# Optimization experiments

Hardware: AMD Instinct MI355X
Metric: run time of the kernel (lower is better)

Reference implementation:

```python
import jax, jax.numpy as jnp
import numpy as np

VOCAB = 50257
EXTRA = 64          # static over-approximation of num_oovs
SEQ = 1024
T_DEC = 100
E = 128
H = 160             # encoder hidden per direction; decoder hidden = 2H = 320
UNK = 3
START = 0
NEG = -1e9


def lstm_cell(x, h, c, wih, whh, bih, bhh):
    # torch gate order: i, f, g, o
    g = x @ wih.T + h @ whh.T + bih + bhh
    i, f, gg, o = jnp.split(g, 4, axis=-1)
    c = jax.nn.sigmoid(f) * c + jax.nn.sigmoid(i) * jnp.tanh(gg)
    h = jax.nn.sigmoid(o) * jnp.tanh(c)
    return h, c


def run_lstm(xs, wih, whh, bih, bhh, hdim):
    def step(carry, x):
        h, c = carry
        h, c = lstm_cell(x, h, c, wih, whh, bih, bhh)
        return (h, c), h
    init = (jnp.zeros((hdim,), xs.dtype), jnp.zeros((hdim,), xs.dtype))
    (hf, _), hs = jax.lax.scan(step, init, xs)
    return hs, hf


def setup_inputs() -> dict:
    key = jax.random.key(0)
    ks = jax.random.split(key, 20)
    rn = lambda k, shape, s: (jax.random.normal(k, shape, dtype=jnp.float32) * s)
    inp = {
        'input_ids': jax.random.randint(ks[0], (SEQ,), 0, VOCAB + EXTRA),
        'embedding': rn(ks[1], (VOCAB, E), 0.1),
        'enc_wih_f': rn(ks[2], (4 * H, E), 0.08),
        'enc_whh_f': rn(ks[3], (4 * H, H), 0.08),
        'enc_bih_f': rn(ks[4], (4 * H,), 0.05),
        'enc_bhh_f': rn(ks[5], (4 * H,), 0.05),
        'enc_wih_b': rn(ks[6], (4 * H, E), 0.08),
        'enc_whh_b': rn(ks[7], (4 * H, H), 0.08),
        'enc_bih_b': rn(ks[8], (4 * H,), 0.05),
        'enc_bhh_b': rn(ks[9], (4 * H,), 0.05),
        'dec_wih': rn(ks[10], (8 * H, E), 0.08),
        'dec_whh': rn(ks[11], (8 * H, 2 * H), 0.08),
        'dec_bih': rn(ks[12], (8 * H,), 0.05),
        'dec_bhh': rn(ks[13], (8 * H,), 0.05),
        'enc_attn_proj': rn(ks[14], (2 * H, 2 * H), 0.02),
        'dec_attn_proj': rn(ks[15], (2 * H, 2 * H), 0.02),
        'vocab_proj': rn(ks[16], (E, 6 * H), 0.05),
        'out_bias': rn(ks[17], (VOCAB,), 0.01),
        'switch_w': rn(ks[18], (1, 6 * H), 0.05),
        'switch_b': rn(ks[19], (1,), 0.05),
    }
    return inp


def reference(input_ids, embedding, enc_wih_f, enc_whh_f, enc_bih_f, enc_bhh_f,
              enc_wih_b, enc_whh_b, enc_bih_b, enc_bhh_b,
              dec_wih, dec_whh, dec_bih, dec_bhh,
              enc_attn_proj, dec_attn_proj, vocab_proj, out_bias,
              switch_w, switch_b):
    ids_in = jnp.where(input_ids >= VOCAB, UNK, input_ids)
    emb = embedding[ids_in]                               # [S, E]

    # bidirectional encoder LSTM
    h_fwd, hfin_f = run_lstm(emb, enc_wih_f, enc_whh_f, enc_bih_f, enc_bhh_f, H)
    h_bwd_rev, hfin_b = run_lstm(emb[::-1], enc_wih_b, enc_whh_b, enc_bih_b, enc_bhh_b, H)
    enc_h = jnp.concatenate([h_fwd, h_bwd_rev[::-1]], axis=-1)   # [S, 2H]

    # step-invariant vocab projection: tanh(W_emb @ vocab_proj) -> [V, 6H]
    out_proj = jnp.tanh(embedding @ vocab_proj)

    # precompute projected encoder states for attention: [S, 2H]
    enc_proj_h = enc_h @ enc_attn_proj.T

    h0 = jnp.concatenate([hfin_f, hfin_b])                # [2H]
    c0 = jnp.zeros((2 * H,), enc_h.dtype)
    dec_buf0 = jnp.zeros((T_DEC, 2 * H), enc_h.dtype)
    cum0 = jnp.zeros((SEQ,), enc_h.dtype)
    tok0 = jnp.asarray(START, dtype=input_ids.dtype)
    t_range = jnp.arange(T_DEC)

    def step(carry, t):
        h, c, cum, dec_buf, tok = carry
        x = embedding[jnp.where(tok >= VOCAB, UNK, tok)]
        h, c = lstm_cell(x, h, c, dec_wih, dec_whh, dec_bih, dec_bhh)

        # intra-temporal encoder attention
        scores = enc_proj_h @ h                           # [S] = h @ W_e @ enc_h.T
        cum_safe = jnp.where(t == 0, 1.0, cum)
        temporal = jnp.where(t == 0, scores, jnp.exp(scores) / cum_safe)
        attn = jax.nn.softmax(temporal)
        enc_ctx = attn @ enc_h                            # [2H]

        # intra-decoder attention over previous decoder hidden states
        dscores = (h @ dec_attn_proj) @ dec_buf.T         # [T_DEC]
        dmask = t_range < t
        dattn = jax.nn.softmax(jnp.where(dmask, dscores, NEG))
        dec_ctx = jnp.where(t == 0, jnp.zeros_like(h), dattn @ dec_buf)

        concat = jnp.concatenate([h, enc_ctx, dec_ctx])   # [6H]
        vocab_dist = jax.nn.softmax(out_proj @ concat + out_bias)  # [V]
        p_copy = jax.nn.sigmoid(jnp.dot(switch_w[0], concat) + switch_b[0])
        gen = jnp.pad((1.0 - p_copy) * vocab_dist, (0, EXTRA))     # [V+EXTRA]
        final = gen.at[input_ids].add(p_copy * attn)      # pointer scatter-add

        cum = cum + scores
        dec_buf = dec_buf.at[t].set(h)
        tok = jnp.argmax(final).astype(input_ids.dtype)   # greedy decode
        return (h, c, cum, dec_buf, tok), final

    _, finals = jax.lax.scan(step, (h0, c0, cum0, dec_buf0, tok0), t_range)
    return finals                                         # [T_DEC, V+EXTRA]
```

## Files before the change

### kernel.cpp

```cpp
#include <hip/hip_runtime.h>
#include <cstdint>

#define VOCAB 50257
#define VTOT  50321
#define TDEC  100
#define UNK   3
#define NBLK  256
#define NTHR  512
#define VB0   17
#define NVB   197
#define K4N   120

static const size_t OFF_WT     = 0;
static const size_t OFF_EMB    = 0;
static const size_t OFF_WIHT_F = 131072;
static const size_t OFF_WIHT_B = 212992;
static const size_t OFF_WTE    = 294912;
static const size_t OFF_XG     = 397312;
static const size_t OFF_ENCH   = 24207360;
static const size_t OFF_EPH    = 24535040;
static const size_t OFF_DECBUF = 24862720;
static const size_t OFF_GATES  = 24894720;
static const size_t OFF_HPAR   = 24896000;
static const size_t OFF_CPAR   = 24898560;
static const size_t OFF_DCTX   = 24903680;
static const size_t OFF_H0     = 24904000;
static const size_t OFF_TEMP   = 24904320;
static const size_t OFF_ATTN   = 24905344;
static const size_t OFF_PMS    = 24906368;
static const size_t OFF_BM     = 24906880;
static const size_t OFF_BS     = 24907136;
static const size_t OFF_AVAL   = 24907392;
static const size_t OFF_AIDX   = 24907648;
static const size_t OFF_PC     = 24907904;
static const size_t OFF_BAR    = 24907968;
static const size_t OFF_SKEY   = 24908032;
static const size_t OFF_SPOS   = 24909056;
static const size_t OFF_BSTART = 24910080;

__device__ __forceinline__ float sigmf(float x) { return 1.f / (1.f + expf(-x)); }

__device__ __forceinline__ float wsum64(float x) {
#pragma unroll
  for (int m = 1; m < 64; m <<= 1) x += __shfl_xor(x, m, 64);
  return x;
}

__device__ __forceinline__ unsigned short bf16r(float x) {
  uint32_t b = __float_as_uint(x);
  uint32_t r = (b + 0x7fffu + ((b >> 16) & 1u)) >> 16;
  return (unsigned short)r;
}
__device__ __forceinline__ float bflo(unsigned u) { return __uint_as_float(u << 16); }
__device__ __forceinline__ float bfhi(unsigned u) { return __uint_as_float(u & 0xffff0000u); }

__device__ __forceinline__ float cload(const float* p) {
  return __hip_atomic_load((float*)p, __ATOMIC_RELAXED, __HIP_MEMORY_SCOPE_AGENT);
}
__device__ __forceinline__ void cstore(float* p, float v) {
  __hip_atomic_store(p, v, __ATOMIC_RELAXED, __HIP_MEMORY_SCOPE_AGENT);
}
__device__ __forceinline__ int cloadi(const int* p) {
  return __hip_atomic_load((int*)p, __ATOMIC_RELAXED, __HIP_MEMORY_SCOPE_AGENT);
}
__device__ __forceinline__ void cstorei(int* p, int v) {
  __hip_atomic_store(p, v, __ATOMIC_RELAXED, __HIP_MEMORY_SCOPE_AGENT);
}

__device__ __forceinline__ void gridbar(float* ws) {
  int* bar = (int*)(ws + OFF_BAR);
  __syncthreads();
  if (threadIdx.x == 0) {
    asm volatile("s_waitcnt vmcnt(0) lgkmcnt(0)" ::: "memory");
    int g = __hip_atomic_load(&bar[32], __ATOMIC_RELAXED, __HIP_MEMORY_SCOPE_AGENT);
    int old = __hip_atomic_fetch_add(&bar[0], 1, __ATOMIC_RELAXED, __HIP_MEMORY_SCOPE_AGENT);
    if (old == NBLK - 1) {
      __hip_atomic_store(&bar[0], 0, __ATOMIC_RELAXED, __HIP_MEMORY_SCOPE_AGENT);
      __hip_atomic_store(&bar[32], g + 1, __ATOMIC_RELAXED, __HIP_MEMORY_SCOPE_AGENT);
    } else {
      while (__hip_atomic_load(&bar[32], __ATOMIC_RELAXED, __HIP_MEMORY_SCOPE_AGENT) == g)
        __builtin_amdgcn_s_sleep(2);
    }
  }
  __syncthreads();
}

__global__ __launch_bounds__(256) void k_setup(float* __restrict__ ws, const int* __restrict__ ids,
                                               const float* __restrict__ embt, const float* __restrict__ ewf,
                                               const float* __restrict__ ewb, const float* __restrict__ eap) {
  int idx = blockIdx.x * 256 + threadIdx.x;
  if (idx < 131072) {
    int tt = idx >> 7, e = idx & 127;
    int id = ids[tt]; if (id >= VOCAB) id = UNK;
    ws[OFF_EMB + idx] = embt[(size_t)id * 128 + e];
  } else if (idx < 212992) {
    int i = idx - 131072;
    int k = i / 640, g = i - (i / 640) * 640;
    ws[OFF_WIHT_F + i] = ewf[(size_t)g * 128 + k];
  } else if (idx < 294912) {
    int i = idx - 212992;
    int k = i / 640, g = i - (i / 640) * 640;
    ws[OFF_WIHT_B + i] = ewb[(size_t)g * 128 + k];
  } else if (idx < 397312) {
    int i = idx - 294912;
    int k = i / 320, j = i - (i / 320) * 320;
    ws[OFF_WTE + i] = eap[(size_t)j * 320 + k];
  }
}

__global__ __launch_bounds__(256) void k_xg(float* __restrict__ ws,
                                            const float* __restrict__ bif, const float* __restrict__ bhf,
                                            const float* __restrict__ bib, const float* __restrict__ bhb) {
  int idx = blockIdx.x * 256 + threadIdx.x;
  int d = idx / 655360;
  int r = idx - d * 655360;
  int tt = r / 640, g = r - (r / 640) * 640;
  const float* wT = ws + (d ? OFF_WIHT_B : OFF_WIHT_F);
  const float* er = ws + OFF_EMB + (size_t)(d ? (1023 - tt) : tt) * 128;
  float acc = d ? (bib[g] + bhb[g]) : (bif[g] + bhf[g]);
#pragma unroll 4
  for (int k = 0; k < 128; ++k) acc += er[k] * wT[(size_t)k * 640 + g];
  ws[OFF_XG + idx] = acc;
}

__global__ __launch_bounds__(512) void k_encoder(float* __restrict__ ws, const float* __restrict__ whh_f,
                                                 const float* __restrict__ whh_b) {
  const int dir = blockIdx.x;
  const int tid = threadIdx.x;
  const float* whh = dir ? whh_b : whh_f;
  const float* xg = ws + OFF_XG + (size_t)dir * 655360;
  __shared__ float hbuf[160];
  __shared__ float part[4][640];
  const int q = tid & 127, kg = tid >> 7, ks = kg * 40;
  float w[5][40];
#pragma unroll
  for (int j = 0; j < 5; ++j)
#pragma unroll
    for (int i = 0; i < 40; ++i)
      w[j][i] = whh[(size_t)(5 * q + j) * 160 + ks + i];
  float cst = 0.f;
  if (tid < 160) hbuf[tid] = 0.f;
  __syncthreads();
  for (int t = 0; t < 1024; ++t) {
    float acc[5] = {0.f, 0.f, 0.f, 0.f, 0.f};
#pragma unroll
    for (int i4 = 0; i4 < 10; ++i4) {
      float4 h4 = *(const float4*)&hbuf[ks + i4 * 4];
#pragma unroll
      for (int j = 0; j < 5; ++j)
        acc[j] += w[j][i4 * 4 + 0] * h4.x + w[j][i4 * 4 + 1] * h4.y + w[j][i4 * 4 + 2] * h4.z + w[j][i4 * 4 + 3] * h4.w;
    }
#pragma unroll
    for (int j = 0; j < 5; ++j) part[kg][5 * q + j] = acc[j];
    __syncthreads();
    if (tid < 160) {
      float gi = xg[(size_t)t * 640 + tid];
      float gf = xg[(size_t)t * 640 + 160 + tid];
      float gg = xg[(size_t)t * 640 + 320 + tid];
      float go = xg[(size_t)t * 640 + 480 + tid];
#pragma unroll
      for (int k2 = 0; k2 < 4; ++k2) {
        gi += part[k2][tid]; gf += part[k2][160 + tid];
        gg += part[k2][320 + tid]; go += part[k2][480 + tid];
      }
      cst = sigmf(gf) * cst + sigmf(gi) * tanhf(gg);
      float hn = sigmf(go) * tanhf(cst);
      hbuf[tid] = hn;
      int trow = dir ? (1023 - t) : t;
      ws[OFF_ENCH + (size_t)trow * 320 + dir * 160 + tid] = hn;
    }
    __syncthreads();
  }
  if (tid < 160) ws[OFF_H0 + dir * 160 + tid] = hbuf[tid];
}

__global__ __launch_bounds__(256) void k_encproj(float* __restrict__ ws) {
  int idx = blockIdx.x * 256 + threadIdx.x;
  int s = idx / 320, j = idx - (idx / 320) * 320;
  const float* er = ws + OFF_ENCH + (size_t)s * 320;
  const float* wt = ws + OFF_WTE;
  float acc = 0.f;
#pragma unroll 4
  for (int k = 0; k < 320; ++k) acc += er[k] * wt[(size_t)k * 320 + j];
  ws[OFF_EPH + idx] = acc;
}

__global__ __launch_bounds__(256) void k_outproj(const float* __restrict__ embt, const float* __restrict__ vp,
                                                 float* __restrict__ ws) {
  __shared__ float As[64][128];
  __shared__ float Bs[128][64];
  __shared__ unsigned T[32][64];
  const int tid = threadIdx.x;
  const int v0 = blockIdx.x * 64, n0 = blockIdx.y * 64;
  for (int c = 0; c < 32; ++c) {
    int idx = c * 256 + tid;
    int m = idx >> 7, k = idx & 127;
    int v = v0 + m;
    As[m][k] = (v < VOCAB) ? embt[(size_t)v * 128 + k] : 0.f;
    int k2 = idx >> 6, n = idx & 63;
    Bs[k2][n] = vp[(size_t)k2 * 960 + n0 + n];
  }
  __syncthreads();
  const int mi = tid >> 4, ni = tid & 15;
  float acc[4][4] = {};
  for (int k = 0; k < 128; ++k) {
    float a0 = As[mi * 4 + 0][k], a1 = As[mi * 4 + 1][k], a2 = As[mi * 4 + 2][k], a3 = As[mi * 4 + 3][k];
    float4 b = *(const float4*)&Bs[k][ni * 4];
    acc[0][0] += a0 * b.x; acc[0][1] += a0 * b.y; acc[0][2] += a0 * b.z; acc[0][3] += a0 * b.w;
    acc[1][0] += a1 * b.x; acc[1][1] += a1 * b.y; acc[1][2] += a1 * b.z; acc[1][3] += a1 * b.w;
    acc[2][0] += a2 * b.x; acc[2][1] += a2 * b.y; acc[2][2] += a2 * b.z; acc[2][3] += a2 * b.w;
    acc[3][0] += a3 * b.x; acc[3][1] += a3 * b.y; acc[3][2] += a3 * b.z; acc[3][3] += a3 * b.w;
  }
#pragma unroll
  for (int i = 0; i < 4; ++i) {
    unsigned p0 = (unsigned)bf16r(tanhf(acc[i][0])) | ((unsigned)bf16r(tanhf(acc[i][1])) << 16);
    unsigned p1 = (unsigned)bf16r(tanhf(acc[i][2])) | ((unsigned)bf16r(tanhf(acc[i][3])) << 16);
    T[2 * ni][mi * 4 + i] = p0;
    T[2 * ni + 1][mi * 4 + i] = p1;
  }
  __syncthreads();
  uint4* WT4 = (uint4*)(ws + OFF_WT);
  const int vb = blockIdx.x >> 2;
  const int rb = (blockIdx.x & 3) * 64;
  const int k4b = n0 >> 3;
#pragma unroll
  for (int i = 0; i < 2; ++i) {
    int flat = i * 256 + tid;
    int k4l = flat >> 6, col = flat & 63;
    uint4 u;
    u.x = T[4 * k4l + 0][col];
    u.y = T[4 * k4l + 1][col];
    u.z = T[4 * k4l + 2][col];
    u.w = T[4 * k4l + 3][col];
    WT4[(size_t)vb * (K4N * 256) + (size_t)(k4b + k4l) * 256 + rb + col] = u;
  }
}

__global__ __launch_bounds__(512) void k_sort(float* __restrict__ ws, const int* __restrict__ ids) {
  __shared__ int sk[1024], sp[1024];
  const int tid = threadIdx.x;
  for (int j = tid; j < 1024; j += 512) { sk[j] = ids[j]; sp[j] = j; }
  __syncthreads();
  for (int k = 2; k <= 1024; k <<= 1)
    for (int j = k >> 1; j > 0; j >>= 1) {
      for (int i = tid; i < 1024; i += 512) {
        int ixj = i ^ j;
        if (ixj > i) {
          bool up = ((i & k) == 0);
          int a = sk[i], b2 = sk[ixj];
          if (up ? (a > b2) : (a < b2)) {
            sk[i] = b2; sk[ixj] = a;
            int pa = sp[i]; sp[i] = sp[ixj]; sp[ixj] = pa;
          }
        }
      }
      __syncthreads();
    }
  int* BST = (int*)(ws + OFF_BSTART);
  int* SK = (int*)(ws + OFF_SKEY);
  int* SP = (int*)(ws + OFF_SPOS);
  for (int j = tid; j < 1024; j += 512) {
    SK[j] = sk[j]; SP[j] = sp[j];
    int o1 = sk[j] >> 8;
    int o0 = (j == 0) ? -1 : (sk[j - 1] >> 8);
    for (int o = o0 + 1; o <= o1; ++o) BST[o] = j;
  }
  if (tid < 256) {
    ws[OFF_AVAL + tid] = -1e30f;
    ((int*)(ws + OFF_AIDX))[tid] = 0;
    ws[OFF_BM + tid] = -1e30f;
    ws[OFF_BS + tid] = 0.f;
  }
  if (tid == 0) {
    int olast = sk[1023] >> 8;
    for (int o = olast + 1; o <= NVB; ++o) BST[o] = 1024;
    int* bar = (int*)(ws + OFF_BAR);
    bar[0] = 0; bar[32] = 0;
  }
}

__global__ __launch_bounds__(512) void k_decode(float* __restrict__ ws, float* __restrict__ out,
    const float* __restrict__ embt,
    const float* __restrict__ dwih, const float* __restrict__ dwhh,
    const float* __restrict__ dbih, const float* __restrict__ dbhh,
    const float* __restrict__ dap, const float* __restrict__ sw,
    const float* __restrict__ sb, const float* __restrict__ ob) {
  const int b = blockIdx.x, tid = threadIdx.x;
  const int l = tid & 63, w = tid >> 6;
  const int rl = tid & 255, half = tid >> 8;
  const int vb = b - VB0;
  const bool isv = (vb >= 0) && (vb < NVB);
  const int vrow = isv ? (vb * 256 + rl) : 0;
  const bool myrow = isv && (vrow < VOCAB);
  const uint4* WTb = ((const uint4*)(ws + OFF_WT)) + (size_t)(isv ? vb : 0) * (K4N * 256) + rl;

  __shared__ __align__(16) float hL[320];
  __shared__ float cL[320];
  __shared__ __align__(16) float concatL[960];
  __shared__ float logitsL[256];
  __shared__ float p0L[256], p1L[256];
  __shared__ float tauL[4], cumL[4];
  __shared__ float redA[512], redB[512];
  __shared__ int   redI[512];
  __shared__ float attnL[64], dsL[128], daL[128], hpL[320];

  if (tid < 320) { hL[tid] = ws[OFF_H0 + tid]; cL[tid] = 0.f; }
  if (tid < 4) cumL[tid] = 0.f;
  __syncthreads();

  for (int t = 0; t < TDEC; ++t) {
    int token = 0;
    if (t > 0) {
      float av = -1e30f; int ai = 0;
      if (tid < 256) { av = cload(&ws[OFF_AVAL + tid]); ai = cloadi(((const int*)(ws + OFF_AIDX)) + tid); }
      redA[tid] = av; redI[tid] = ai;
      __syncthreads();
      for (int off = 256; off > 0; off >>= 1) {
        if (tid < off) {
          float v2 = redA[tid + off]; int i2 = redI[tid + off];
          if (v2 > redA[tid] || (v2 == redA[tid] && i2 < redI[tid])) { redA[tid] = v2; redI[tid] = i2; }
        }
        __syncthreads();
      }
      token = redI[0];
    }
    int tokm = (token >= VOCAB) ? UNK : token;
    if (w < 5) {
      const int r = 5 * b + w;
      float acc = dwih[(size_t)r * 128 + l] * embt[(size_t)tokm * 128 + l]
                + dwih[(size_t)r * 128 + 64 + l] * embt[(size_t)tokm * 128 + 64 + l];
#pragma unroll
      for (int c = 0; c < 5; ++c) acc += dwhh[(size_t)r * 320 + c * 64 + l] * hL[c * 64 + l];
      acc = wsum64(acc);
      if (l == 0) cstore(&ws[OFF_GATES + r], acc + dbih[r] + dbhh[r]);
    }
    gridbar(ws);

    if (tid < 320) {
      float gi = cload(&ws[OFF_GATES + tid]);
      float gf = cload(&ws[OFF_GATES + 320 + tid]);
      float gg = cload(&ws[OFF_GATES + 640 + tid]);
      float go = cload(&ws[OFF_GATES + 960 + tid]);
      float c = sigmf(gf) * cL[tid] + sigmf(gi) * tanhf(gg);
      cL[tid] = c;
      float hn = sigmf(go) * tanhf(c);
      hL[tid] = hn;
      if (b == 16) ws[OFF_DECBUF + (size_t)t * 320 + tid] = hn;
    }
    __syncthreads();
    if (w < 4) {
      const int srow = 4 * b + w;
      const float* er = ws + OFF_EPH + (size_t)srow * 320;
      float acc = 0.f;
#pragma unroll
      for (int c = 0; c < 5; ++c) acc += er[c * 64 + l] * hL[c * 64 + l];
      acc = wsum64(acc);
      float tau = (t == 0) ? acc : expf(acc) / cumL[w];
      if (l == 0) {
        tauL[w] = tau;
        cstore(&ws[OFF_TEMP + srow], tau);
        cumL[w] += acc;
      }
    }
    if (b < 8 && tid < 320) {
      float acc = 0.f;
#pragma unroll 8
      for (int ii = 0; ii < 40; ++ii) {
        int i = b * 40 + ii;
        acc += hL[i] * dap[(size_t)i * 320 + tid];
      }
      cstore(&ws[OFF_HPAR + b * 320 + tid], acc);
    }
    __syncthreads();
    if (tid == 0) {
      float m4 = fmaxf(fmaxf(tauL[0], tauL[1]), fmaxf(tauL[2], tauL[3]));
      float s4 = expf(tauL[0] - m4) + expf(tauL[1] - m4) + expf(tauL[2] - m4) + expf(tauL[3] - m4);
      cstore(&ws[OFF_PMS + 2 * b], m4);
      cstore(&ws[OFF_PMS + 2 * b + 1], s4);
    }
    gridbar(ws);

    float ga0 = 0.f, ga1 = 0.f;
    if (b < 16) {
      float m = -1e30f, s = 0.f;
      if (tid < 256) { m = cload(&ws[OFF_PMS + 2 * tid]); s = cload(&ws[OFF_PMS + 2 * tid + 1]); }
      redA[tid] = m; redB[tid] = s;
      __syncthreads();
      for (int off = 256; off > 0; off >>= 1) {
        if (tid < off) {
          float m1 = redA[tid], m2 = redA[tid + off];
          float mx = fmaxf(m1, m2);
          redB[tid] = redB[tid] * expf(m1 - mx) + redB[tid + off] * expf(m2 - mx);
          redA[tid] = mx;
        }
        __syncthreads();
      }
      const float M = redA[0], S = redB[0];
      __syncthreads();
      if (tid < 64) {
        float a = expf(cload(&ws[OFF_TEMP + 64 * b + tid]) - M) / S;
        attnL[tid] = a;
        cstore(&ws[OFF_ATTN + 64 * b + tid], a);
      }
      __syncthreads();
      if (tid < 320) {
        float acc = 0.f;
        const float* eh = ws + OFF_ENCH + (size_t)(64 * b) * 320 + tid;
#pragma unroll 4
        for (int k2 = 0; k2 < 64; ++k2) acc += attnL[k2] * eh[(size_t)k2 * 320];
        cstore(&ws[OFF_CPAR + b * 320 + tid], acc);
      }
    } else if (b == 16) {
      if (tid < 320) {
        float a = 0.f;
#pragma unroll
        for (int q = 0; q < 8; ++q) a += cload(&ws[OFF_HPAR + q * 320 + tid]);
        hpL[tid] = a;
      }
      __syncthreads();
      float hpv[5];
#pragma unroll
      for (int c = 0; c < 5; ++c) hpv[c] = hpL[c * 64 + l];
#pragma unroll
      for (int k2 = 0; k2 < 13; ++k2) {
        int tp = w + 8 * k2;
        if (tp < t) {
          float acc = 0.f;
#pragma unroll
          for (int c = 0; c < 5; ++c) acc += hpv[c] * ws[OFF_DECBUF + (size_t)tp * 320 + c * 64 + l];
          acc = wsum64(acc);
          if (l == 0) dsL[tp] = acc;
        }
      }
      __syncthreads();
      float dv = -1e30f;
      if (tid < 128) { dv = (tid < t) ? dsL[tid] : -1e30f; redA[tid] = dv; }
      __syncthreads();
      for (int off = 64; off > 0; off >>= 1) { if (tid < off) redA[tid] = fmaxf(redA[tid], redA[tid + off]); __syncthreads(); }
      float dmx = redA[0];
      __syncthreads();
      float de = (tid < 128) ? expf(dv - dmx) : 0.f;
      if (tid < 128) redA[tid] = de;
      __syncthreads();
      for (int off = 64; off > 0; off >>= 1) { if (tid < off) redA[tid] += redA[tid + off]; __syncthreads(); }
      float dS = redA[0];
      __syncthreads();
      if (tid < 128) daL[tid] = de / dS;
      __syncthreads();
      if (tid < 320) {
        float acc = 0.f;
        for (int tp = 0; tp < t; ++tp) acc += daL[tp] * ws[OFF_DECBUF + (size_t)tp * 320 + tid];
        cstore(&ws[OFF_DCTX + tid], (t == 0) ? 0.f : acc);
      }
    } else if (isv) {
      const int c0 = half ? 20 : 0;
#pragma unroll 10
      for (int k4 = c0; k4 < c0 + 20; ++k4) {
        uint4 u = WTb[(size_t)k4 * 256];
        float4 fa = *(const float4*)&hL[8 * k4];
        float4 fb = *(const float4*)&hL[8 * k4 + 4];
        ga0 += bflo(u.x) * fa.x + bflo(u.y) * fa.z + bflo(u.z) * fb.x + bflo(u.w) * fb.z;
        ga1 += bfhi(u.x) * fa.y + bfhi(u.y) * fa.w + bfhi(u.z) * fb.y + bfhi(u.w) * fb.w;
      }
    }
    gridbar(ws);

    if (isv || b == 0) {
      if (tid < 320) {
        float e = 0.f;
#pragma unroll
        for (int g2 = 0; g2 < 16; ++g2) e += cload(&ws[OFF_CPAR + g2 * 320 + tid]);
        concatL[tid] = hL[tid];
        concatL[320 + tid] = e;
        concatL[640 + tid] = cload(&ws[OFF_DCTX + tid]);
      }
    }
    __syncthreads();
    if (b == 0 && w == 0) {
      float acc = 0.f;
#pragma unroll
      for (int c = 0; c < 15; ++c) acc += sw[c * 64 + l] * concatL[c * 64 + l];
      acc = wsum64(acc);
      if (l == 0) cstore(&ws[OFF_PC], 1.f / (1.f + expf(-(acc + sb[0]))));
    }
    if (isv) {
      const int d0 = half ? 80 : 40;
#pragma unroll 8
      for (int k4 = d0; k4 < d0 + 40; ++k4) {
        uint4 u = WTb[(size_t)k4 * 256];
        float4 fa = *(const float4*)&concatL[8 * k4];
        float4 fb = *(const float4*)&concatL[8 * k4 + 4];
        ga0 += bflo(u.x) * fa.x + bflo(u.y) * fa.z + bflo(u.z) * fb.x + bflo(u.w) * fb.z;
        ga1 += bfhi(u.x) * fa.y + bfhi(u.y) * fa.w + bfhi(u.z) * fb.y + bfhi(u.w) * fb.w;
      }
      if (half) p1L[rl] = ga0 + ga1; else p0L[rl] = ga0 + ga1;
    }
    __syncthreads();
    float lm = -1e30f, ls = 0.f;
    if (isv && tid < 256) {
      float lv = myrow ? (p0L[tid] + p1L[tid] + ob[vrow]) : -1e30f;
      logitsL[tid] = lv;
      if (lv > -1e29f) { lm = lv; ls = 1.f; }
    }
    redA[tid] = lm; redB[tid] = ls;
    __syncthreads();
    for (int off = 256; off > 0; off >>= 1) {
      if (tid < off) {
        float m1 = redA[tid], m2 = redA[tid + off];
        float mx = fmaxf(m1, m2);
        redB[tid] = redB[tid] * expf(m1 - mx) + redB[tid + off] * expf(m2 - mx);
        redA[tid] = mx;
      }
      __syncthreads();
    }
    if (isv && tid == 0) { cstore(&ws[OFF_BM + vb], redA[0]); cstore(&ws[OFF_BS + vb], redB[0]); }
    gridbar(ws);

    if (isv) {
      float m = -1e30f, s = 0.f;
      if (tid < 256) { m = cload(&ws[OFF_BM + tid]); s = cload(&ws[OFF_BS + tid]); }
      redA[tid] = m; redB[tid] = s;
      __syncthreads();
      for (int off = 256; off > 0; off >>= 1) {
        if (tid < off) {
          float m1 = redA[tid], m2 = redA[tid + off];
          float mx = fmaxf(m1, m2);
          redB[tid] = redB[tid] * expf(m1 - mx) + redB[tid + off] * expf(m2 - mx);
          redA[tid] = mx;
        }
        __syncthreads();
      }
      const float M = redA[0], Sg = redB[0];
      const float pc = cload(&ws[OFF_PC]);
      const float scale = (1.f - pc) / Sg;
      __syncthreads();
      const int* BST = (const int*)(ws + OFF_BSTART);
      const int* SK = (const int*)(ws + OFF_SKEY);
      const int* SP = (const int*)(ws + OFF_SPOS);
      bool act = (tid < 256) && (vrow < VTOT);
      float val = -1e30f;
      if (act) {
        val = (vrow < VOCAB) ? scale * expf(logitsL[tid] - M) : 0.f;
        int jb = BST[vb], je = BST[vb + 1];
        for (int j = jb; j < je; ++j)
          if (SK[j] == vrow) val += pc * cload(&ws[OFF_ATTN + SP[j]]);
        out[(size_t)t * VTOT + vrow] = val;
      }
      redA[tid] = act ? val : -1e30f; redI[tid] = vrow;
      __syncthreads();
      for (int off = 256; off > 0; off >>= 1) {
        if (tid < off) {
          float v2 = redA[tid + off]; int i2 = redI[tid + off];
          if (v2 > redA[tid] || (v2 == redA[tid] && i2 < redI[tid])) { redA[tid] = v2; redI[tid] = i2; }
        }
        __syncthreads();
      }
      if (tid == 0) { cstore(&ws[OFF_AVAL + b], redA[0]); cstorei(((int*)(ws + OFF_AIDX)) + b, redI[0]); }
    }
    gridbar(ws);
  }
}

extern "C" void kernel_launch(void* const* d_in, const int* in_sizes, int n_in,
                              void* d_out, int out_size, void* d_ws, size_t ws_size,
                              hipStream_t stream) {
  const int*   ids  = (const int*)d_in[0];
  const float* embt = (const float*)d_in[1];
  const float* ewf  = (const float*)d_in[2];
  const float* ehf  = (const float*)d_in[3];
  const float* ebif = (const float*)d_in[4];
  const float* ebhf = (const float*)d_in[5];
  const float* ewb  = (const float*)d_in[6];
  const float* ehb  = (const float*)d_in[7];
  const float* ebib = (const float*)d_in[8];
  const float* ebhb = (const float*)d_in[9];
  const float* dwih = (const float*)d_in[10];
  const float* dwhh = (const float*)d_in[11];
  const float* dbih = (const float*)d_in[12];
  const float* dbhh = (const float*)d_in[13];
  const float* eap  = (const float*)d_in[14];
  const float* dap  = (const float*)d_in[15];
  const float* vp   = (const float*)d_in[16];
  const float* ob   = (const float*)d_in[17];
  const float* sw   = (const float*)d_in[18];
  const float* sb   = (const float*)d_in[19];
  float* out = (float*)d_out;
  float* ws  = (float*)d_ws;

  k_setup<<<1558, 256, 0, stream>>>(ws, ids, embt, ewf, ewb, eap);
  k_xg<<<5120, 256, 0, stream>>>(ws, ebif, ebhf, ebib, ebhb);
  k_encoder<<<2, 512, 0, stream>>>(ws, ehf, ehb);
  k_encproj<<<1280, 256, 0, stream>>>(ws);
  k_outproj<<<dim3(786, 15), 256, 0, stream>>>(embt, vp, ws);
  k_sort<<<1, 512, 0, stream>>>(ws, ids);
  k_decode<<<NBLK, NTHR, 0, stream>>>(ws, out, embt, dwih, dwhh, dbih, dbhh, dap, sw, sb, ob);
}
```

Measured before the change: 8.535 ms.

## Spread vocab projection over all blocks, prefetch weights, use hierarchical grid barrier

Reassigns the vocabulary projection so every one of the 256 persistent blocks owns 200 vocab rows, instead of 197 blocks owning 256 rows while 17 blocks do attention and other work. Each block's slice of the bf16 weight layout is loaded into registers before the barriers and attention phases, so weight fetch latency overlaps with other work. The single-counter grid barrier becomes a two-level barrier: 16 groups of 16 blocks each count locally, then one top-level counter releases all groups. This costs more registers per thread and puts vocab work on the attention blocks, which can lengthen their critical path.

```diff
diff --git a/kernel.cpp b/kernel.cpp
--- a/kernel.cpp
+++ b/kernel.cpp
@@ -7,36 +7,36 @@
 #define UNK   3
 #define NBLK  256
 #define NTHR  512
-#define VB0   17
-#define NVB   197
-#define K4N   120
-
-static const size_t OFF_WT     = 0;
+#define VPB   200
+#define NSL   252
+#define K4SL  24000
+
 static const size_t OFF_EMB    = 0;
 static const size_t OFF_WIHT_F = 131072;
 static const size_t OFF_WIHT_B = 212992;
 static const size_t OFF_WTE    = 294912;
 static const size_t OFF_XG     = 397312;
-static const size_t OFF_ENCH   = 24207360;
-static const size_t OFF_EPH    = 24535040;
-static const size_t OFF_DECBUF = 24862720;
-static const size_t OFF_GATES  = 24894720;
-static const size_t OFF_HPAR   = 24896000;
-static const size_t OFF_CPAR   = 24898560;
-static const size_t OFF_DCTX   = 24903680;
-static const size_t OFF_H0     = 24904000;
-static const size_t OFF_TEMP   = 24904320;
-static const size_t OFF_ATTN   = 24905344;
-static const size_t OFF_PMS    = 24906368;
-static const size_t OFF_BM     = 24906880;
-static const size_t OFF_BS     = 24907136;
-static const size_t OFF_AVAL   = 24907392;
-static const size_t OFF_AIDX   = 24907648;
-static const size_t OFF_PC     = 24907904;
-static const size_t OFF_BAR    = 24907968;
-static const size_t OFF_SKEY   = 24908032;
-static const size_t OFF_SPOS   = 24909056;
-static const size_t OFF_BSTART = 24910080;
+static const size_t OFF_WT     = 294912;
+static const size_t OFF_ENCH   = 24486912;
+static const size_t OFF_EPH    = 24814592;
+static const size_t OFF_DECBUF = 25142272;
+static const size_t OFF_GATES  = 25174272;
+static const size_t OFF_HPAR   = 25175552;
+static const size_t OFF_CPAR   = 25178112;
+static const size_t OFF_DCTX   = 25183232;
+static const size_t OFF_H0     = 25183552;
+static const size_t OFF_TEMP   = 25183872;
+static const size_t OFF_ATTN   = 25184896;
+static const size_t OFF_PMS    = 25185920;
+static const size_t OFF_BM     = 25186432;
+static const size_t OFF_BS     = 25186688;
+static const size_t OFF_AVAL   = 25186944;
+static const size_t OFF_AIDX   = 25187200;
+static const size_t OFF_PC     = 25187456;
+static const size_t OFF_BAR    = 25187520;
+static const size_t OFF_SKEY   = 25189568;
+static const size_t OFF_SPOS   = 25190592;
+static const size_t OFF_BSTART = 25191616;
 
 __device__ __forceinline__ float sigmf(float x) { return 1.f / (1.f + expf(-x)); }
 
@@ -67,20 +67,25 @@
   __hip_atomic_store(p, v, __ATOMIC_RELAXED, __HIP_MEMORY_SCOPE_AGENT);
 }
 
-__device__ __forceinline__ void gridbar(float* ws) {
+__device__ __forceinline__ void gridbar(float* ws, int b) {
   int* bar = (int*)(ws + OFF_BAR);
   __syncthreads();
   if (threadIdx.x == 0) {
     asm volatile("s_waitcnt vmcnt(0) lgkmcnt(0)" ::: "memory");
-    int g = __hip_atomic_load(&bar[32], __ATOMIC_RELAXED, __HIP_MEMORY_SCOPE_AGENT);
-    int old = __hip_atomic_fetch_add(&bar[0], 1, __ATOMIC_RELAXED, __HIP_MEMORY_SCOPE_AGENT);
-    if (old == NBLK - 1) {
-      __hip_atomic_store(&bar[0], 0, __ATOMIC_RELAXED, __HIP_MEMORY_SCOPE_AGENT);
-      __hip_atomic_store(&bar[32], g + 1, __ATOMIC_RELAXED, __HIP_MEMORY_SCOPE_AGENT);
-    } else {
-      while (__hip_atomic_load(&bar[32], __ATOMIC_RELAXED, __HIP_MEMORY_SCOPE_AGENT) == g)
-        __builtin_amdgcn_s_sleep(2);
-    }
+    const int g = b >> 4;
+    int* ggen = &bar[512 + g * 32];
+    int myg = __hip_atomic_load(ggen, __ATOMIC_RELAXED, __HIP_MEMORY_SCOPE_AGENT);
+    int old = __hip_atomic_fetch_add(&bar[g * 32], 1, __ATOMIC_RELAXED, __HIP_MEMORY_SCOPE_AGENT);
+    if ((old & 15) == 15) {
+      int r = __hip_atomic_fetch_add(&bar[1024], 1, __ATOMIC_RELAXED, __HIP_MEMORY_SCOPE_AGENT);
+      if ((r & 15) == 15) {
+#pragma unroll
+        for (int i = 0; i < 16; ++i)
+          __hip_atomic_store(&bar[512 + i * 32], myg + 1, __ATOMIC_RELAXED, __HIP_MEMORY_SCOPE_AGENT);
+      }
+    }
+    while (__hip_atomic_load(ggen, __ATOMIC_RELAXED, __HIP_MEMORY_SCOPE_AGENT) == myg)
+      __builtin_amdgcn_s_sleep(1);
   }
   __syncthreads();
 }
@@ -220,19 +225,22 @@
   }
   __syncthreads();
   uint4* WT4 = (uint4*)(ws + OFF_WT);
-  const int vb = blockIdx.x >> 2;
-  const int rb = (blockIdx.x & 3) * 64;
   const int k4b = n0 >> 3;
 #pragma unroll
   for (int i = 0; i < 2; ++i) {
     int flat = i * 256 + tid;
     int k4l = flat >> 6, col = flat & 63;
-    uint4 u;
-    u.x = T[4 * k4l + 0][col];
-    u.y = T[4 * k4l + 1][col];
-    u.z = T[4 * k4l + 2][col];
-    u.w = T[4 * k4l + 3][col];
-    WT4[(size_t)vb * (K4N * 256) + (size_t)(k4b + k4l) * 256 + rb + col] = u;
+    int v = v0 + col;
+    if (v < VOCAB) {
+      int vb = v / VPB;
+      int rl = v - vb * VPB;
+      uint4 u;
+      u.x = T[4 * k4l + 0][col];
+      u.y = T[4 * k4l + 1][col];
+      u.z = T[4 * k4l + 2][col];
+      u.w = T[4 * k4l + 3][col];
+      WT4[(size_t)vb * K4SL + (size_t)(k4b + k4l) * VPB + rl] = u;
+    }
   }
 }
 
@@ -261,10 +269,11 @@
   int* SP = (int*)(ws + OFF_SPOS);
   for (int j = tid; j < 1024; j += 512) {
     SK[j] = sk[j]; SP[j] = sp[j];
-    int o1 = sk[j] >> 8;
-    int o0 = (j == 0) ? -1 : (sk[j - 1] >> 8);
+    int o1 = sk[j] / VPB;
+    int o0 = (j == 0) ? -1 : (sk[j - 1] / VPB);
     for (int o = o0 + 1; o <= o1; ++o) BST[o] = j;
   }
+  for (int j = tid; j < 2048; j += 512) ((int*)(ws + OFF_BAR))[j] = 0;
   if (tid < 256) {
     ws[OFF_AVAL + tid] = -1e30f;
     ((int*)(ws + OFF_AIDX))[tid] = 0;
@@ -272,12 +281,18 @@
     ws[OFF_BS + tid] = 0.f;
   }
   if (tid == 0) {
-    int olast = sk[1023] >> 8;
-    for (int o = olast + 1; o <= NVB; ++o) BST[o] = 1024;
-    int* bar = (int*)(ws + OFF_BAR);
-    bar[0] = 0; bar[32] = 0;
-  }
-}
+    int olast = sk[1023] / VPB;
+    for (int o = olast + 1; o <= 256; ++o) BST[o] = 1024;
+  }
+}
+
+#define LDB(dst, kb) { _Pragma("unroll") for (int j = 0; j < 10; ++j) dst[j] = WTb[(size_t)((kb) + j) * VPB]; }
+#define ACCW(src, kb, CV) { _Pragma("unroll") for (int j = 0; j < 10; ++j) { \
+    const int kk = (kb) + j; \
+    float4 fa = *(const float4*)&CV[8 * kk]; \
+    float4 fb = *(const float4*)&CV[8 * kk + 4]; \
+    ga0 += bflo(src[j].x) * fa.x + bflo(src[j].y) * fa.z + bflo(src[j].z) * fb.x + bflo(src[j].w) * fb.z; \
+    ga1 += bfhi(src[j].x) * fa.y + bfhi(src[j].y) * fa.w + bfhi(src[j].z) * fb.y + bfhi(src[j].w) * fb.w; } }
 
 __global__ __launch_bounds__(512) void k_decode(float* __restrict__ ws, float* __restrict__ out,
     const float* __restrict__ embt,
@@ -288,11 +303,10 @@
   const int b = blockIdx.x, tid = threadIdx.x;
   const int l = tid & 63, w = tid >> 6;
   const int rl = tid & 255, half = tid >> 8;
-  const int vb = b - VB0;
-  const bool isv = (vb >= 0) && (vb < NVB);
-  const int vrow = isv ? (vb * 256 + rl) : 0;
-  const bool myrow = isv && (vrow < VOCAB);
-  const uint4* WTb = ((const uint4*)(ws + OFF_WT)) + (size_t)(isv ? vb : 0) * (K4N * 256) + rl;
+  const int vrow = b * VPB + rl;
+  const bool act = (rl < VPB) && (vrow < VOCAB);
+  const bool hasout = (b * VPB) < VTOT;
+  const uint4* WTb = ((const uint4*)(ws + OFF_WT)) + (size_t)b * K4SL + rl;
 
   __shared__ __align__(16) float hL[320];
   __shared__ float cL[320];
@@ -334,7 +348,7 @@
       acc = wsum64(acc);
       if (l == 0) cstore(&ws[OFF_GATES + r], acc + dbih[r] + dbhh[r]);
     }
-    gridbar(ws);
+    gridbar(ws, b);
 
     if (tid < 320) {
       float gi = cload(&ws[OFF_GATES + tid]);
@@ -378,9 +392,11 @@
       cstore(&ws[OFF_PMS + 2 * b], m4);
       cstore(&ws[OFF_PMS + 2 * b + 1], s4);
     }
-    gridbar(ws);
-
-    float ga0 = 0.f, ga1 = 0.f;
+    gridbar(ws, b);
+
+    uint4 wA[10], wB[10];
+    const int c0 = half ? 20 : 0;
+    if (act) { LDB(wA, c0); LDB(wB, c0 + 10); }
     if (b < 16) {
       float m = -1e30f, s = 0.f;
       if (tid < 256) { m = cload(&ws[OFF_PMS + 2 * tid]); s = cload(&ws[OFF_PMS + 2 * tid + 1]); }
@@ -452,28 +468,20 @@
         for (int tp = 0; tp < t; ++tp) acc += daL[tp] * ws[OFF_DECBUF + (size_t)tp * 320 + tid];
         cstore(&ws[OFF_DCTX + tid], (t == 0) ? 0.f : acc);
       }
-    } else if (isv) {
-      const int c0 = half ? 20 : 0;
-#pragma unroll 10
-      for (int k4 = c0; k4 < c0 + 20; ++k4) {
-        uint4 u = WTb[(size_t)k4 * 256];
-        float4 fa = *(const float4*)&hL[8 * k4];
-        float4 fb = *(const float4*)&hL[8 * k4 + 4];
-        ga0 += bflo(u.x) * fa.x + bflo(u.y) * fa.z + bflo(u.z) * fb.x + bflo(u.w) * fb.z;
-        ga1 += bfhi(u.x) * fa.y + bfhi(u.y) * fa.w + bfhi(u.z) * fb.y + bfhi(u.w) * fb.w;
-      }
-    }
-    gridbar(ws);
-
-    if (isv || b == 0) {
-      if (tid < 320) {
-        float e = 0.f;
-#pragma unroll
-        for (int g2 = 0; g2 < 16; ++g2) e += cload(&ws[OFF_CPAR + g2 * 320 + tid]);
-        concatL[tid] = hL[tid];
-        concatL[320 + tid] = e;
-        concatL[640 + tid] = cload(&ws[OFF_DCTX + tid]);
-      }
+    }
+    float ga0 = 0.f, ga1 = 0.f;
+    if (act) { ACCW(wA, c0, hL); ACCW(wB, c0 + 10, hL); }
+    gridbar(ws, b);
+
+    const int d0 = half ? 80 : 40;
+    if (act) { LDB(wA, d0); LDB(wB, d0 + 10); }
+    if (tid < 320) {
+      float e = 0.f;
+#pragma unroll
+      for (int g2 = 0; g2 < 16; ++g2) e += cload(&ws[OFF_CPAR + g2 * 320 + tid]);
+      concatL[tid] = hL[tid];
+      concatL[320 + tid] = e;
+      concatL[640 + tid] = cload(&ws[OFF_DCTX + tid]);
     }
     __syncthreads();
     if (b == 0 && w == 0) {
@@ -483,43 +491,22 @@
       acc = wsum64(acc);
       if (l == 0) cstore(&ws[OFF_PC], 1.f / (1.f + expf(-(acc + sb[0]))));
     }
-    if (isv) {
-      const int d0 = half ? 80 : 40;
-#pragma unroll 8
-      for (int k4 = d0; k4 < d0 + 40; ++k4) {
-        uint4 u = WTb[(size_t)k4 * 256];
-        float4 fa = *(const float4*)&concatL[8 * k4];
-        float4 fb = *(const float4*)&concatL[8 * k4 + 4];
-        ga0 += bflo(u.x) * fa.x + bflo(u.y) * fa.z + bflo(u.z) * fb.x + bflo(u.w) * fb.z;
-        ga1 += bfhi(u.x) * fa.y + bfhi(u.y) * fa.w + bfhi(u.z) * fb.y + bfhi(u.w) * fb.w;
-      }
+    if (act) {
+      ACCW(wA, d0, concatL); LDB(wA, d0 + 20);
+      ACCW(wB, d0 + 10, concatL); LDB(wB, d0 + 30);
+      ACCW(wA, d0 + 20, concatL);
+      ACCW(wB, d0 + 30, concatL);
       if (half) p1L[rl] = ga0 + ga1; else p0L[rl] = ga0 + ga1;
     }
     __syncthreads();
-    float lm = -1e30f, ls = 0.f;
-    if (isv && tid < 256) {
-      float lv = myrow ? (p0L[tid] + p1L[tid] + ob[vrow]) : -1e30f;
-      logitsL[tid] = lv;
-      if (lv > -1e29f) { lm = lv; ls = 1.f; }
-    }
-    redA[tid] = lm; redB[tid] = ls;
-    __syncthreads();
-    for (int off = 256; off > 0; off >>= 1) {
-      if (tid < off) {
-        float m1 = redA[tid], m2 = redA[tid + off];
-        float mx = fmaxf(m1, m2);
-        redB[tid] = redB[tid] * expf(m1 - mx) + redB[tid + off] * expf(m2 - mx);
-        redA[tid] = mx;
-      }
-      __syncthreads();
-    }
-    if (isv && tid == 0) { cstore(&ws[OFF_BM + vb], redA[0]); cstore(&ws[OFF_BS + vb], redB[0]); }
-    gridbar(ws);
-
-    if (isv) {
-      float m = -1e30f, s = 0.f;
-      if (tid < 256) { m = cload(&ws[OFF_BM + tid]); s = cload(&ws[OFF_BS + tid]); }
-      redA[tid] = m; redB[tid] = s;
+    {
+      float lm = -1e30f, ls = 0.f;
+      if (tid < VPB) {
+        float lv = (vrow < VOCAB) ? (p0L[tid] + p1L[tid] + ob[vrow]) : -1e30f;
+        logitsL[tid] = lv;
+        if (lv > -1e29f) { lm = lv; ls = 1.f; }
+      }
+      redA[tid] = lm; redB[tid] = ls;
       __syncthreads();
       for (int off = 256; off > 0; off >>= 1) {
         if (tid < off) {
@@ -530,23 +517,41 @@
         }
         __syncthreads();
       }
+      if (tid == 0 && hasout) { cstore(&ws[OFF_BM + b], redA[0]); cstore(&ws[OFF_BS + b], redB[0]); }
+    }
+    gridbar(ws, b);
+
+    {
+      float m = -1e30f, s = 0.f;
+      if (tid < 256) { m = cload(&ws[OFF_BM + tid]); s = cload(&ws[OFF_BS + tid]); }
+      redA[tid] = m; redB[tid] = s;
+      __syncthreads();
+      for (int off = 256; off > 0; off >>= 1) {
+        if (tid < off) {
+          float m1 = redA[tid], m2 = redA[tid + off];
+          float mx = fmaxf(m1, m2);
+          redB[tid] = redB[tid] * expf(m1 - mx) + redB[tid + off] * expf(m2 - mx);
+          redA[tid] = mx;
+        }
+        __syncthreads();
+      }
       const float M = redA[0], Sg = redB[0];
       const float pc = cload(&ws[OFF_PC]);
       const float scale = (1.f - pc) / Sg;
       __syncthreads();
-      const int* BST = (const int*)(ws + OFF_BSTART);
-      const int* SK = (const int*)(ws + OFF_SKEY);
-      const int* SP = (const int*)(ws + OFF_SPOS);
-      bool act = (tid < 256) && (vrow < VTOT);
+      bool acte = (tid < VPB) && (vrow < VTOT);
       float val = -1e30f;
-      if (act) {
+      if (acte) {
         val = (vrow < VOCAB) ? scale * expf(logitsL[tid] - M) : 0.f;
-        int jb = BST[vb], je = BST[vb + 1];
+        const int* BST = (const int*)(ws + OFF_BSTART);
+        const int* SK = (const int*)(ws + OFF_SKEY);
+        const int* SP = (const int*)(ws + OFF_SPOS);
+        int jb = BST[b], je = BST[b + 1];
         for (int j = jb; j < je; ++j)
           if (SK[j] == vrow) val += pc * cload(&ws[OFF_ATTN + SP[j]]);
         out[(size_t)t * VTOT + vrow] = val;
       }
-      redA[tid] = act ? val : -1e30f; redI[tid] = vrow;
+      redA[tid] = acte ? val : -1e30f; redI[tid] = vrow;
       __syncthreads();
       for (int off = 256; off > 0; off >>= 1) {
         if (tid < off) {
@@ -555,9 +560,9 @@
         }
         __syncthreads();
       }
-      if (tid == 0) { cstore(&ws[OFF_AVAL + b], redA[0]); cstorei(((int*)(ws + OFF_AIDX)) + b, redI[0]); }
-    }
-    gridbar(ws);
+      if (tid == 0 && hasout) { cstore(&ws[OFF_AVAL + b], redA[0]); cstorei(((int*)(ws + OFF_AIDX)) + b, redI[0]); }
+    }
+    gridbar(ws, b);
   }
 }
 
@@ -587,7 +592,7 @@
   float* out = (float*)d_out;
   float* ws  = (float*)d_ws;
 
-  k_setup<<<1558, 256, 0, stream>>>(ws, ids, embt, ewf, ewb, eap);
+  k_setup<<<1552, 256, 0, stream>>>(ws, ids, embt, ewf, ewb, eap);
   k_xg<<<5120, 256, 0, stream>>>(ws, ebif, ebhf, ebib, ebhb);
   k_encoder<<<2, 512, 0, stream>>>(ws, ehf, ehb);
   k_encproj<<<1280, 256, 0, stream>>>(ws);
```

After: 10.65 ms. 1.25x slower.
